# Kernel optimization log

Measured on AMD Instinct MI355X. Metric: run time of the kernel, lower is better.

Reference implementation:

```python
import jax, jax.numpy as jnp
import numpy as np

N = 8192
H = 64
ALPHA = 0.2
NEG_INF = -9e15


def gru_cell(x, h, w_ih, w_hh, b_ih, b_hh):
    # PyTorch GRUCell: gates ordered (r, z, n)
    gi = x @ w_ih.T + b_ih  # [N, 3H]
    gh = h @ w_hh.T + b_hh
    ir, iz, inn = jnp.split(gi, 3, axis=1)
    hr, hz, hn = jnp.split(gh, 3, axis=1)
    r = jax.nn.sigmoid(ir + hr)
    z = jax.nn.sigmoid(iz + hz)
    n = jnp.tanh(inn + r * hn)
    return (1.0 - z) * n + z * h


def gat(h, node_adj, edge_adj, W, a):
    hw = h @ W  # [N, H]
    h_plus = (node_adj > 0).astype(hw.dtype) @ hw
    h_minus = (node_adj < 0).astype(hw.dtype) @ hw
    # a: [2H, 1] -> per-row scalar scores
    e_plus = jax.nn.leaky_relu(jnp.concatenate([h_plus, h_minus], axis=1) @ a, ALPHA)   # [N,1]
    e_minus = jax.nn.leaky_relu(jnp.concatenate([h_minus, h_plus], axis=1) @ a, ALPHA)  # [N,1]
    # broadcast [N,1] over columns == torch .repeat(1, N)
    att = jnp.where(edge_adj > 0, e_plus, NEG_INF)
    att = jnp.where(edge_adj < 0, e_minus, att)
    att = jax.nn.softmax(att, axis=1)
    return (att * edge_adj) @ hw  # concat=False -> no elu


def setup_inputs() -> dict:
    key = jax.random.key(0)
    ks = jax.random.split(key, 12)
    f32 = jnp.float32
    inp = {
        "h": jax.random.normal(ks[0], (N, H), f32),
        "node_adj": jax.random.normal(ks[1], (N, N), f32),
        "edge_adj": jax.random.normal(ks[2], (N, N), f32),
        # GAT params
        "W_gat": jax.random.normal(ks[3], (H, H), f32) * (1.414 * np.sqrt(6.0 / (2 * H))),
        "a_gat": jax.random.normal(ks[4], (2 * H, 1), f32) * (1.414 * np.sqrt(6.0 / (2 * H + 1))),
        # edge GRU (msg_type='concat' -> input 2H)
        "w_ih_e": jax.random.normal(ks[5], (3 * H, 2 * H), f32) * 0.01,
        "w_hh_e": jax.random.normal(ks[6], (3 * H, H), f32) * 0.01,
        "b_ih_e": jnp.zeros((3 * H,), f32),
        "b_hh_e": jnp.zeros((3 * H,), f32),
        # node GRU
        "w_ih_n": jax.random.normal(ks[7], (3 * H, H), f32) * 0.01,
        "w_hh_n": jax.random.normal(ks[8], (3 * H, H), f32) * 0.01,
        "b_ih_n": jnp.zeros((3 * H,), f32),
        "b_hh_n": jnp.zeros((3 * H,), f32),
    }
    return inp


def reference(h, node_adj, edge_adj, W_gat, a_gat,
              w_ih_e, w_hh_e, b_ih_e, b_hh_e,
              w_ih_n, w_hh_n, b_ih_n, b_hh_n):
    d_node = jnp.diag(node_adj)  # diag(I_node)
    d_edge = jnp.diag(edge_adj)
    A_node = node_adj - jnp.diag(d_node)  # node_adj - I_node
    A_edge = edge_adj - jnp.diag(d_edge)
    # msg_type == 'concat'
    node_support = jnp.concatenate(
        [(A_node > 0).astype(h.dtype) @ h, (A_node < 0).astype(h.dtype) @ h], axis=1)
    edge_output = gru_cell(node_support, h, w_ih_e, w_hh_e, b_ih_e, b_hh_e)
    edge_support = gat(h, A_node, A_edge, W_gat, a_gat)
    node_output = gru_cell(edge_support, h, w_ih_n, w_hh_n, b_ih_n, b_hh_n)
    # mm with diagonal matrices == row scaling
    return d_edge[:, None] * edge_output + d_node[:, None] * node_output
```

## Files before the change

kernel.cpp:

```cpp
#include <hip/hip_runtime.h>

#define NN 8192
#define HH 64
constexpr float LALPHA = 0.2f;

typedef __attribute__((ext_vector_type(8))) short bf16x8;
typedef __attribute__((ext_vector_type(4))) float f32x4;

__device__ inline short f2bf(float f) {
  unsigned u = __builtin_bit_cast(unsigned, f);
  u += 0x7FFFu + ((u >> 16) & 1u);
  return (short)(u >> 16);
}

__global__ __launch_bounds__(256) void k_prep(const float* __restrict__ h,
                                              const float* __restrict__ na,
                                              const float* __restrict__ ea,
                                              unsigned short* __restrict__ ht,
                                              float* __restrict__ dn,
                                              float* __restrict__ de,
                                              float* __restrict__ HbP) {
  __shared__ float tile[64][65];
  const int j0 = blockIdx.x * 64;
  for (int l = threadIdx.x; l < 64 * 64; l += 256) {
    int r = l >> 6, c = l & 63;
    tile[r][c] = h[(size_t)(j0 + r) * HH + c];
  }
  __syncthreads();
  for (int l = threadIdx.x; l < 64 * 64; l += 256) {
    int c = l >> 6, r = l & 63;
    ht[(size_t)c * NN + j0 + r] = (unsigned short)f2bf(tile[r][c]);
  }
  const int t = threadIdx.x;
  if (t < 64) {
    float s = 0.f;
    for (int r = 0; r < 64; ++r) s += tile[r][t];
    HbP[blockIdx.x * 64 + t] = s;
  } else if (t < 128) {
    int i = j0 + (t - 64);
    dn[i] = na[(size_t)i * NN + i];
    de[i] = ea[(size_t)i * NN + i];
  }
}

__global__ __launch_bounds__(256) void k_wprep(
    const float* __restrict__ W, const float* __restrict__ ag,
    const float* __restrict__ wihe, const float* __restrict__ whhe,
    const float* __restrict__ wihn, const float* __restrict__ whhn,
    const float* __restrict__ HbP, float* __restrict__ Hb,
    float* __restrict__ wa0, float* __restrict__ wa1,
    float* __restrict__ wihTe, float* __restrict__ whhTe,
    float* __restrict__ WnT, float* __restrict__ whhTn) {
  const int bid = blockIdx.x, t = threadIdx.x;
  if (bid == 64) {
    __shared__ float sW[64][64];
    __shared__ float sa[128];
    for (int l = t; l < 4096; l += 256) sW[l >> 6][l & 63] = W[l];
    if (t < 128) sa[t] = ag[t];
    __syncthreads();
    if (t < 64) {
      float s0 = 0.f, s1 = 0.f;
      for (int j = 0; j < 64; ++j) {
        s0 += sW[t][j] * sa[j];
        s1 += sW[t][j] * sa[64 + j];
      }
      wa0[t] = s0;
      wa1[t] = s1;
    } else if (t < 128) {
      int c = t - 64;
      float s = 0.f;
      for (int b = 0; b < 128; ++b) s += HbP[b * 64 + c];
      Hb[c] = s;
    }
    return;
  }
  for (int x = bid * 256 + t; x < 49152; x += 64 * 256) {
    if (x < 24576) {
      int k = x / 192, g = x % 192;
      wihTe[x] = wihe[g * 128 + k];
    } else if (x < 36864) {
      int o = x - 24576, k = o / 192, g = o % 192;
      whhTe[o] = whhe[g * 64 + k];
    } else {
      int o = x - 36864, k = o / 192, g = o % 192;
      whhTn[o] = whhn[g * 64 + k];
    }
  }
  if (bid < 48) {
    const int o = bid * 256 + t;
    const int k = o / 192, g = o % 192;
    float s = 0.f;
    for (int j = 0; j < 64; ++j) s += wihn[g * 64 + j] * W[k * 64 + j];
    WnT[o] = s;
  }
}

template <int KS>
__global__ __launch_bounds__(256, 4) void k_stageA(
    const float* __restrict__ na, const float* __restrict__ ea,
    const unsigned short* __restrict__ ht,
    float* __restrict__ SpP, float* __restrict__ TfP,
    float* __restrict__ TpP, float* __restrict__ cpP) {
  const int lane  = threadIdx.x & 63;
  const int wid   = threadIdx.x >> 6;
  const int row16 = lane & 15;
  const int kgrp  = lane >> 4;
  const int i0    = blockIdx.x * 64 + wid * 16;
  const int ks    = blockIdx.y;
  const int kbeg  = ks * (NN / KS);
  constexpr int ITERS = NN / KS / 32;
  const int start = blockIdx.x & (ITERS - 1);

  f32x4 accS[4] = {}, accF[4] = {}, accP[4] = {};
  float cnt = 0.f;

  const float* naRow = na + (size_t)(i0 + row16) * NN;
  const float* eaRow = ea + (size_t)(i0 + row16) * NN;

  for (int it = 0; it < ITERS; ++it) {
    int tt = start + it;
    if (tt >= ITERS) tt -= ITERS;
    const int kk = kbeg + tt * 32 + kgrp * 8;
    const float4 a0 = *reinterpret_cast<const float4*>(naRow + kk);
    const float4 a1 = *reinterpret_cast<const float4*>(naRow + kk + 4);
    const float4 e0 = *reinterpret_cast<const float4*>(eaRow + kk);
    const float4 e1 = *reinterpret_cast<const float4*>(eaRow + kk + 4);
    const float av[8] = {a0.x, a0.y, a0.z, a0.w, a1.x, a1.y, a1.z, a1.w};
    const float ev[8] = {e0.x, e0.y, e0.z, e0.w, e1.x, e1.y, e1.z, e1.w};
    bf16x8 fS, fF, fP;
#pragma unroll
    for (int q = 0; q < 8; ++q) {
      fS[q] = (av[q] > 0.f) ? (short)0x3F80 : (short)0;
      fF[q] = f2bf(ev[q]);
      fP[q] = f2bf(fmaxf(ev[q], 0.f));
      cnt += (ev[q] > 0.f) ? 1.f : 0.f;
    }
#pragma unroll
    for (int c = 0; c < 4; ++c) {
      const bf16x8 fB = *reinterpret_cast<const bf16x8*>(
          ht + (size_t)(c * 16 + row16) * NN + kk);
      accS[c] = __builtin_amdgcn_mfma_f32_16x16x32_bf16(fS, fB, accS[c], 0, 0, 0);
      accF[c] = __builtin_amdgcn_mfma_f32_16x16x32_bf16(fF, fB, accF[c], 0, 0, 0);
      accP[c] = __builtin_amdgcn_mfma_f32_16x16x32_bf16(fP, fB, accP[c], 0, 0, 0);
    }
  }
  cnt += __shfl_xor(cnt, 16);
  cnt += __shfl_xor(cnt, 32);
  if (lane < 16) cpP[ks * NN + i0 + lane] = cnt;

  const size_t base = (size_t)ks * ((size_t)NN * HH);
#pragma unroll
  for (int c = 0; c < 4; ++c) {
#pragma unroll
    for (int r = 0; r < 4; ++r) {
      const int row = i0 + kgrp * 4 + r;
      const int col = c * 16 + row16;
      const size_t idx = base + (size_t)row * HH + col;
      SpP[idx] = accS[c][r];
      TfP[idx] = accF[c][r];
      TpP[idx] = accP[c][r];
    }
  }
}

template <int KSP>
__global__ __launch_bounds__(256) void k_epi(
    const float* __restrict__ h, const float* __restrict__ dn_g,
    const float* __restrict__ de_g, const float* __restrict__ Hb,
    const float* __restrict__ SpP, const float* __restrict__ TfP,
    const float* __restrict__ TpP, const float* __restrict__ cpP,
    const float* __restrict__ wa0, const float* __restrict__ wa1,
    const float* __restrict__ wihTe, const float* __restrict__ whhTe,
    const float* __restrict__ bihe, const float* __restrict__ bhhe,
    const float* __restrict__ WnT, const float* __restrict__ whhTn,
    const float* __restrict__ bihn, const float* __restrict__ bhhn,
    float* __restrict__ out) {
  __shared__ float xs[16][128];
  __shared__ float hs[16][64];
  __shared__ float us[16][64];
  __shared__ float eos[16][64];
  __shared__ float sHb[64], sw0[64], sw1[64];
  const int t = threadIdx.x;
  const int lane = t & 63, w = t >> 6;
  const int i0 = blockIdx.x * 16;
  const size_t SZ = (size_t)NN * HH;

  if (t < 64) {
    sHb[t] = Hb[t];
    sw0[t] = wa0[t];
    sw1[t] = wa1[t];
  }
  {
    const int row = t >> 4, c4 = (t & 15) * 4;
    *reinterpret_cast<float4*>(&hs[row][c4]) =
        *reinterpret_cast<const float4*>(&h[(size_t)(i0 + row) * 64 + c4]);
  }
  __syncthreads();

  for (int rr = 0; rr < 4; ++rr) {
    const int row = w * 4 + rr;
    const size_t idx = (size_t)(i0 + row) * 64 + lane;
    float sp = 0.f, tf = 0.f, tp = 0.f;
#pragma unroll
    for (int s = 0; s < KSP; ++s) {
      sp += SpP[s * SZ + idx];
      tf += TfP[s * SZ + idx];
      tp += TpP[s * SZ + idx];
    }
    const float hv = hs[row][lane];
    const float dni = dn_g[i0 + row], dei = de_g[i0 + row];
    sp -= (dni > 0.f) ? hv : 0.f;
    tf -= dei * hv;
    tp -= fmaxf(dei, 0.f) * hv;
    const float sm = sHb[lane] - hv - sp;
    const float tm = tf - tp;
    float cp = 0.f;
#pragma unroll
    for (int s = 0; s < KSP; ++s) cp += cpP[s * NN + i0 + row];
    cp -= (dei > 0.f) ? 1.f : 0.f;
    float ep = sp * sw0[lane] + sm * sw1[lane];
    float em = sm * sw0[lane] + sp * sw1[lane];
#pragma unroll
    for (int off = 32; off >= 1; off >>= 1) {
      ep += __shfl_xor(ep, off);
      em += __shfl_xor(em, off);
    }
    ep = ep > 0.f ? ep : LALPHA * ep;
    em = em > 0.f ? em : LALPHA * em;
    const float cm = (float)(NN - 1) - cp;
    const float NEGI = -3.0e38f;
    const float m = fmaxf(cp > 0.f ? ep : NEGI, cm > 0.f ? em : NEGI);
    const float xp = (cp > 0.f) ? expf(ep - m) : 0.f;
    const float xm = (cm > 0.f) ? expf(em - m) : 0.f;
    const float den = cp * xp + cm * xm;
    const float inv = den > 0.f ? 1.f / den : 0.f;
    xs[row][lane] = sp;
    xs[row][64 + lane] = sm;
    us[row][lane] = xp * inv * tp + xm * inv * tm;
  }
  __syncthreads();

  {
    const int c = lane;
    float gi[3][4] = {}, gh[3][4] = {};
    for (int k = 0; k < 128; ++k) {
      const float wr = wihTe[k * 192 + c], wz = wihTe[k * 192 + 64 + c],
                  wn = wihTe[k * 192 + 128 + c];
#pragma unroll
      for (int rr = 0; rr < 4; ++rr) {
        const float x = xs[w * 4 + rr][k];
        gi[0][rr] += x * wr;
        gi[1][rr] += x * wz;
        gi[2][rr] += x * wn;
      }
    }
    for (int k = 0; k < 64; ++k) {
      const float ur = whhTe[k * 192 + c], uz = whhTe[k * 192 + 64 + c],
                  un = whhTe[k * 192 + 128 + c];
#pragma unroll
      for (int rr = 0; rr < 4; ++rr) {
        const float hv = hs[w * 4 + rr][k];
        gh[0][rr] += hv * ur;
        gh[1][rr] += hv * uz;
        gh[2][rr] += hv * un;
      }
    }
    const float br = bihe[c], bz = bihe[64 + c], bn = bihe[128 + c];
    const float dr = bhhe[c], dz = bhhe[64 + c], dnb = bhhe[128 + c];
#pragma unroll
    for (int rr = 0; rr < 4; ++rr) {
      const int row = w * 4 + rr;
      const float rg = 1.f / (1.f + expf(-(gi[0][rr] + br + gh[0][rr] + dr)));
      const float zg = 1.f / (1.f + expf(-(gi[1][rr] + bz + gh[1][rr] + dz)));
      const float ng = tanhf(gi[2][rr] + bn + rg * (gh[2][rr] + dnb));
      eos[row][c] = (1.f - zg) * ng + zg * hs[row][c];
    }
  }
  __syncthreads();

  {
    const int c = lane;
    float gi[3][4] = {}, gh[3][4] = {};
    for (int k = 0; k < 64; ++k) {
      const float wr = WnT[k * 192 + c], wz = WnT[k * 192 + 64 + c],
                  wn = WnT[k * 192 + 128 + c];
      const float ur = whhTn[k * 192 + c], uz = whhTn[k * 192 + 64 + c],
                  un = whhTn[k * 192 + 128 + c];
#pragma unroll
      for (int rr = 0; rr < 4; ++rr) {
        const float x = us[w * 4 + rr][k], hv = hs[w * 4 + rr][k];
        gi[0][rr] += x * wr;
        gi[1][rr] += x * wz;
        gi[2][rr] += x * wn;
        gh[0][rr] += hv * ur;
        gh[1][rr] += hv * uz;
        gh[2][rr] += hv * un;
      }
    }
    const float br = bihn[c], bz = bihn[64 + c], bn = bihn[128 + c];
    const float dr = bhhn[c], dz = bhhn[64 + c], dnb = bhhn[128 + c];
#pragma unroll
    for (int rr = 0; rr < 4; ++rr) {
      const int row = w * 4 + rr;
      const float rg = 1.f / (1.f + expf(-(gi[0][rr] + br + gh[0][rr] + dr)));
      const float zg = 1.f / (1.f + expf(-(gi[1][rr] + bz + gh[1][rr] + dz)));
      const float ng = tanhf(gi[2][rr] + bn + rg * (gh[2][rr] + dnb));
      const float no = (1.f - zg) * ng + zg * hs[row][c];
      out[(size_t)(i0 + row) * 64 + c] =
          de_g[i0 + row] * eos[row][c] + dn_g[i0 + row] * no;
    }
  }
}

template <int KSP>
static void launch_all(const float* h, const float* na, const float* ea,
                       const float* Wg, const float* ag, const float* wihe,
                       const float* whhe, const float* bihe, const float* bhhe,
                       const float* wihn, const float* whhn, const float* bihn,
                       const float* bhhn, float* out, float* ws,
                       hipStream_t stream) {
  const size_t SZ = (size_t)NN * HH;
  float* SpP = ws;
  float* TfP = ws + (size_t)KSP * SZ;
  float* TpP = ws + (size_t)2 * KSP * SZ;
  float* cpP = ws + (size_t)3 * KSP * SZ;
  float* dn = cpP + (size_t)KSP * NN;
  float* de = dn + NN;
  float* HbP = de + NN;
  float* Hb = HbP + 8192;
  float* wa0 = Hb + 64;
  float* wa1 = wa0 + 64;
  float* wihTe = wa1 + 64;
  float* whhTe = wihTe + 24576;
  float* WnT = whhTe + 12288;
  float* whhTn = WnT + 12288;
  unsigned short* ht = (unsigned short*)(whhTn + 12288);

  k_prep<<<NN / 64, 256, 0, stream>>>(h, na, ea, ht, dn, de, HbP);
  k_wprep<<<65, 256, 0, stream>>>(Wg, ag, wihe, whhe, wihn, whhn, HbP, Hb, wa0,
                                  wa1, wihTe, whhTe, WnT, whhTn);
  k_stageA<KSP><<<dim3(NN / 64, KSP), 256, 0, stream>>>(na, ea, ht, SpP, TfP,
                                                        TpP, cpP);
  k_epi<KSP><<<NN / 16, 256, 0, stream>>>(h, dn, de, Hb, SpP, TfP, TpP, cpP,
                                          wa0, wa1, wihTe, whhTe, bihe, bhhe,
                                          WnT, whhTn, bihn, bhhn, out);
}

extern "C" void kernel_launch(void* const* d_in, const int* in_sizes, int n_in,
                              void* d_out, int out_size, void* d_ws, size_t ws_size,
                              hipStream_t stream) {
  const float* h    = (const float*)d_in[0];
  const float* na   = (const float*)d_in[1];
  const float* ea   = (const float*)d_in[2];
  const float* Wg   = (const float*)d_in[3];
  const float* ag   = (const float*)d_in[4];
  const float* wihe = (const float*)d_in[5];
  const float* whhe = (const float*)d_in[6];
  const float* bihe = (const float*)d_in[7];
  const float* bhhe = (const float*)d_in[8];
  const float* wihn = (const float*)d_in[9];
  const float* whhn = (const float*)d_in[10];
  const float* bihn = (const float*)d_in[11];
  const float* bhhn = (const float*)d_in[12];
  float* out = (float*)d_out;
  float* ws  = (float*)d_ws;

  const size_t SZ = (size_t)NN * HH;
  auto need = [&](int ks) {
    return (3 * (size_t)ks * SZ + (size_t)ks * NN + 2 * NN + 8192 + 192 +
            24576 + 3 * 12288) * 4 + (size_t)NN * HH * 2;
  };
  if (ws_size >= need(8)) {
    launch_all<8>(h, na, ea, Wg, ag, wihe, whhe, bihe, bhhe, wihn, whhn,
                  bihn, bhhn, out, ws, stream);
  } else if (ws_size >= need(4)) {
    launch_all<4>(h, na, ea, Wg, ag, wihe, whhe, bihe, bhhe, wihn, whhn,
                  bihn, bhhn, out, ws, stream);
  } else {
    launch_all<2>(h, na, ea, Wg, ag, wihe, whhe, bihe, bhhe, wihn, whhn,
                  bihn, bhhn, out, ws, stream);
  }
}
```

Measured before the change: 225.7 us.

## Precompress adjacency into bitmask and bf16 before the MFMA stage

Adds a pre-pass kernel that turns node_adj into a 1-bit sign mask and edge_adj into bf16, and counts positive edges per row with atomics. The main MFMA stage then reads the compressed operands and no longer converts fp32 per element. A fallback path keeps fp32 inputs but switches to an atomic positive-count buffer. The aim is to take conversion work out of the matmul loop, but the pre-pass adds a full extra read of both matrices plus roughly 136MB of writes and re-reads per call.

```diff
diff --git a/kernel.cpp b/kernel.cpp
--- a/kernel.cpp
+++ b/kernel.cpp
@@ -19,7 +19,8 @@
                                               unsigned short* __restrict__ ht,
                                               float* __restrict__ dn,
                                               float* __restrict__ de,
-                                              float* __restrict__ HbP) {
+                                              float* __restrict__ HbP,
+                                              int* __restrict__ cpI) {
   __shared__ float tile[64][65];
   const int j0 = blockIdx.x * 64;
   for (int l = threadIdx.x; l < 64 * 64; l += 256) {
@@ -36,10 +37,55 @@
     float s = 0.f;
     for (int r = 0; r < 64; ++r) s += tile[r][t];
     HbP[blockIdx.x * 64 + t] = s;
+    cpI[j0 + t] = 0;
   } else if (t < 128) {
     int i = j0 + (t - 64);
     dn[i] = na[(size_t)i * NN + i];
     de[i] = ea[(size_t)i * NN + i];
+    cpI[j0 + (t - 64) + 0] = 0;
+  }
+  if (t < 64) {  }
+  else if (t >= 192) { cpI[j0 + (t - 192)] = 0; }
+}
+
+__global__ __launch_bounds__(256) void k_prep2(const float* __restrict__ na,
+                                               const float* __restrict__ ea,
+                                               unsigned char* __restrict__ mask,
+                                               unsigned short* __restrict__ ebf,
+                                               int* __restrict__ cpI) {
+  const long long NG = (long long)NN * NN / 8;
+  const int half = gridDim.x >> 1;
+  const bool isNA = (int)blockIdx.x < half;
+  const long long b0 = (long long)(isNA ? blockIdx.x : blockIdx.x - half);
+  const long long stride = (long long)half * 256;
+  for (long long g = b0 * 256 + threadIdx.x; g < NG; g += stride) {
+    if (isNA) {
+      const f32x4 v0 = *reinterpret_cast<const f32x4*>(na + g * 8);
+      const f32x4 v1 = *reinterpret_cast<const f32x4*>(na + g * 8 + 4);
+      unsigned m = 0;
+#pragma unroll
+      for (int q = 0; q < 4; ++q) {
+        m |= (v0[q] > 0.f) ? (1u << q) : 0u;
+        m |= (v1[q] > 0.f) ? (1u << (q + 4)) : 0u;
+      }
+      mask[g] = (unsigned char)m;
+    } else {
+      const f32x4 v0 = *reinterpret_cast<const f32x4*>(ea + g * 8);
+      const f32x4 v1 = *reinterpret_cast<const f32x4*>(ea + g * 8 + 4);
+      bf16x8 o;
+      int tot = 0;
+#pragma unroll
+      for (int q = 0; q < 4; ++q) {
+        o[q] = f2bf(v0[q]);
+        o[q + 4] = f2bf(v1[q]);
+        tot += (v0[q] > 0.f) ? 1 : 0;
+        tot += (v1[q] > 0.f) ? 1 : 0;
+      }
+      *reinterpret_cast<bf16x8*>(ebf + g * 8) = o;
+#pragma unroll
+      for (int off = 32; off >= 1; off >>= 1) tot += __shfl_xor(tot, off);
+      if ((threadIdx.x & 63) == 0) atomicAdd(&cpI[(int)(g >> 10)], tot);
+    }
   }
 }
 
@@ -96,11 +142,10 @@
 }
 
 template <int KS>
-__global__ __launch_bounds__(256, 4) void k_stageA(
-    const float* __restrict__ na, const float* __restrict__ ea,
+__global__ __launch_bounds__(256, 4) void k_stageB(
+    const unsigned char* __restrict__ mask, const unsigned short* __restrict__ ebf,
     const unsigned short* __restrict__ ht,
-    float* __restrict__ SpP, float* __restrict__ TfP,
-    float* __restrict__ TpP, float* __restrict__ cpP) {
+    float* __restrict__ SpP, float* __restrict__ TfP, float* __restrict__ TpP) {
   const int lane  = threadIdx.x & 63;
   const int wid   = threadIdx.x >> 6;
   const int row16 = lane & 15;
@@ -112,29 +157,23 @@
   const int start = blockIdx.x & (ITERS - 1);
 
   f32x4 accS[4] = {}, accF[4] = {}, accP[4] = {};
-  float cnt = 0.f;
-
-  const float* naRow = na + (size_t)(i0 + row16) * NN;
-  const float* eaRow = ea + (size_t)(i0 + row16) * NN;
+
+  const unsigned char* mRow = mask + (size_t)(i0 + row16) * (NN / 8) + (kbeg >> 3) + kgrp;
+  const unsigned short* eRow = ebf + (size_t)(i0 + row16) * NN + kbeg + kgrp * 8;
 
   for (int it = 0; it < ITERS; ++it) {
     int tt = start + it;
     if (tt >= ITERS) tt -= ITERS;
+    const unsigned mb = mRow[tt * 4];
+    const bf16x8 fF = *reinterpret_cast<const bf16x8*>(eRow + tt * 32);
+    bf16x8 fS, fP;
+#pragma unroll
+    for (int q = 0; q < 8; ++q) {
+      fS[q] = ((mb >> q) & 1u) ? (short)0x3F80 : (short)0;
+      const short sv = fF[q];
+      fP[q] = (sv > 0) ? sv : (short)0;
+    }
     const int kk = kbeg + tt * 32 + kgrp * 8;
-    const float4 a0 = *reinterpret_cast<const float4*>(naRow + kk);
-    const float4 a1 = *reinterpret_cast<const float4*>(naRow + kk + 4);
-    const float4 e0 = *reinterpret_cast<const float4*>(eaRow + kk);
-    const float4 e1 = *reinterpret_cast<const float4*>(eaRow + kk + 4);
-    const float av[8] = {a0.x, a0.y, a0.z, a0.w, a1.x, a1.y, a1.z, a1.w};
-    const float ev[8] = {e0.x, e0.y, e0.z, e0.w, e1.x, e1.y, e1.z, e1.w};
-    bf16x8 fS, fF, fP;
-#pragma unroll
-    for (int q = 0; q < 8; ++q) {
-      fS[q] = (av[q] > 0.f) ? (short)0x3F80 : (short)0;
-      fF[q] = f2bf(ev[q]);
-      fP[q] = f2bf(fmaxf(ev[q], 0.f));
-      cnt += (ev[q] > 0.f) ? 1.f : 0.f;
-    }
 #pragma unroll
     for (int c = 0; c < 4; ++c) {
       const bf16x8 fB = *reinterpret_cast<const bf16x8*>(
@@ -144,9 +183,6 @@
       accP[c] = __builtin_amdgcn_mfma_f32_16x16x32_bf16(fP, fB, accP[c], 0, 0, 0);
     }
   }
-  cnt += __shfl_xor(cnt, 16);
-  cnt += __shfl_xor(cnt, 32);
-  if (lane < 16) cpP[ks * NN + i0 + lane] = cnt;
 
   const size_t base = (size_t)ks * ((size_t)NN * HH);
 #pragma unroll
@@ -168,7 +204,7 @@
     const float* __restrict__ h, const float* __restrict__ dn_g,
     const float* __restrict__ de_g, const float* __restrict__ Hb,
     const float* __restrict__ SpP, const float* __restrict__ TfP,
-    const float* __restrict__ TpP, const float* __restrict__ cpP,
+    const float* __restrict__ TpP, const int* __restrict__ cpI,
     const float* __restrict__ wa0, const float* __restrict__ wa1,
     const float* __restrict__ wihTe, const float* __restrict__ whhTe,
     const float* __restrict__ bihe, const float* __restrict__ bhhe,
@@ -214,9 +250,7 @@
     tp -= fmaxf(dei, 0.f) * hv;
     const float sm = sHb[lane] - hv - sp;
     const float tm = tf - tp;
-    float cp = 0.f;
-#pragma unroll
-    for (int s = 0; s < KSP; ++s) cp += cpP[s * NN + i0 + row];
+    float cp = (float)cpI[i0 + row];
     cp -= (dei > 0.f) ? 1.f : 0.f;
     float ep = sp * sw0[lane] + sm * sw1[lane];
     float em = sm * sw0[lane] + sp * sw1[lane];
@@ -312,38 +346,116 @@
   }
 }
 
-template <int KSP>
-static void launch_all(const float* h, const float* na, const float* ea,
-                       const float* Wg, const float* ag, const float* wihe,
-                       const float* whhe, const float* bihe, const float* bhhe,
-                       const float* wihn, const float* whhn, const float* bihn,
-                       const float* bhhn, float* out, float* ws,
-                       hipStream_t stream) {
+template <int KS>
+__global__ __launch_bounds__(256, 4) void k_stageAf(
+    const float* __restrict__ na, const float* __restrict__ ea,
+    const unsigned short* __restrict__ ht,
+    float* __restrict__ SpP, float* __restrict__ TfP,
+    float* __restrict__ TpP, int* __restrict__ cpI) {
+  const int lane  = threadIdx.x & 63;
+  const int wid   = threadIdx.x >> 6;
+  const int row16 = lane & 15;
+  const int kgrp  = lane >> 4;
+  const int i0    = blockIdx.x * 64 + wid * 16;
+  const int ks    = blockIdx.y;
+  const int kbeg  = ks * (NN / KS);
+  constexpr int ITERS = NN / KS / 32;
+  const int start = blockIdx.x & (ITERS - 1);
+
+  f32x4 accS[4] = {}, accF[4] = {}, accP[4] = {};
+  float cnt = 0.f;
+  const float* naRow = na + (size_t)(i0 + row16) * NN;
+  const float* eaRow = ea + (size_t)(i0 + row16) * NN;
+
+  for (int it = 0; it < ITERS; ++it) {
+    int tt = start + it;
+    if (tt >= ITERS) tt -= ITERS;
+    const int kk = kbeg + tt * 32 + kgrp * 8;
+    const float4 a0 = *reinterpret_cast<const float4*>(naRow + kk);
+    const float4 a1 = *reinterpret_cast<const float4*>(naRow + kk + 4);
+    const float4 e0 = *reinterpret_cast<const float4*>(eaRow + kk);
+    const float4 e1 = *reinterpret_cast<const float4*>(eaRow + kk + 4);
+    const float av[8] = {a0.x, a0.y, a0.z, a0.w, a1.x, a1.y, a1.z, a1.w};
+    const float ev[8] = {e0.x, e0.y, e0.z, e0.w, e1.x, e1.y, e1.z, e1.w};
+    bf16x8 fS, fF, fP;
+#pragma unroll
+    for (int q = 0; q < 8; ++q) {
+      fS[q] = (av[q] > 0.f) ? (short)0x3F80 : (short)0;
+      fF[q] = f2bf(ev[q]);
+      fP[q] = f2bf(fmaxf(ev[q], 0.f));
+      cnt += (ev[q] > 0.f) ? 1.f : 0.f;
+    }
+#pragma unroll
+    for (int c = 0; c < 4; ++c) {
+      const bf16x8 fB = *reinterpret_cast<const bf16x8*>(
+          ht + (size_t)(c * 16 + row16) * NN + kk);
+      accS[c] = __builtin_amdgcn_mfma_f32_16x16x32_bf16(fS, fB, accS[c], 0, 0, 0);
+      accF[c] = __builtin_amdgcn_mfma_f32_16x16x32_bf16(fF, fB, accF[c], 0, 0, 0);
+      accP[c] = __builtin_amdgcn_mfma_f32_16x16x32_bf16(fP, fB, accP[c], 0, 0, 0);
+    }
+  }
+  cnt += __shfl_xor(cnt, 16);
+  cnt += __shfl_xor(cnt, 32);
+  if (lane < 16) atomicAdd(&cpI[i0 + lane], (int)cnt);
+
+  const size_t base = (size_t)ks * ((size_t)NN * HH);
+#pragma unroll
+  for (int c = 0; c < 4; ++c) {
+#pragma unroll
+    for (int r = 0; r < 4; ++r) {
+      const int row = i0 + kgrp * 4 + r;
+      const int col = c * 16 + row16;
+      const size_t idx = base + (size_t)row * HH + col;
+      SpP[idx] = accS[c][r];
+      TfP[idx] = accF[c][r];
+      TpP[idx] = accP[c][r];
+    }
+  }
+}
+
+struct WsLayout {
+  float *SpP, *TfP, *TpP, *dn, *de, *HbP, *Hb, *wa0, *wa1, *wihTe, *whhTe, *WnT, *whhTn;
+  int* cpI;
+  unsigned short* ht;
+  unsigned char* mask;
+  unsigned short* ebf;
+};
+
+static WsLayout carve(void* ws, int KS) {
   const size_t SZ = (size_t)NN * HH;
-  float* SpP = ws;
-  float* TfP = ws + (size_t)KSP * SZ;
-  float* TpP = ws + (size_t)2 * KSP * SZ;
-  float* cpP = ws + (size_t)3 * KSP * SZ;
-  float* dn = cpP + (size_t)KSP * NN;
-  float* de = dn + NN;
-  float* HbP = de + NN;
-  float* Hb = HbP + 8192;
-  float* wa0 = Hb + 64;
-  float* wa1 = wa0 + 64;
-  float* wihTe = wa1 + 64;
-  float* whhTe = wihTe + 24576;
-  float* WnT = whhTe + 12288;
-  float* whhTn = WnT + 12288;
-  unsigned short* ht = (unsigned short*)(whhTn + 12288);
-
-  k_prep<<<NN / 64, 256, 0, stream>>>(h, na, ea, ht, dn, de, HbP);
-  k_wprep<<<65, 256, 0, stream>>>(Wg, ag, wihe, whhe, wihn, whhn, HbP, Hb, wa0,
-                                  wa1, wihTe, whhTe, WnT, whhTn);
-  k_stageA<KSP><<<dim3(NN / 64, KSP), 256, 0, stream>>>(na, ea, ht, SpP, TfP,
-                                                        TpP, cpP);
-  k_epi<KSP><<<NN / 16, 256, 0, stream>>>(h, dn, de, Hb, SpP, TfP, TpP, cpP,
-                                          wa0, wa1, wihTe, whhTe, bihe, bhhe,
-                                          WnT, whhTn, bihn, bhhn, out);
+  uintptr_t p = (uintptr_t)ws;
+  auto take = [&](size_t bytes) {
+    uintptr_t r = (p + 255) & ~(uintptr_t)255;
+    p = r + bytes;
+    return r;
+  };
+  WsLayout L;
+  L.SpP = (float*)take(KS * SZ * 4);
+  L.TfP = (float*)take(KS * SZ * 4);
+  L.TpP = (float*)take(KS * SZ * 4);
+  L.dn = (float*)take(NN * 4);
+  L.de = (float*)take(NN * 4);
+  L.HbP = (float*)take(8192 * 4);
+  L.Hb = (float*)take(64 * 4);
+  L.wa0 = (float*)take(64 * 4);
+  L.wa1 = (float*)take(64 * 4);
+  L.wihTe = (float*)take(24576 * 4);
+  L.whhTe = (float*)take(12288 * 4);
+  L.WnT = (float*)take(12288 * 4);
+  L.whhTn = (float*)take(12288 * 4);
+  L.cpI = (int*)take(NN * 4);
+  L.ht = (unsigned short*)take((size_t)NN * 64 * 2);
+  L.mask = (unsigned char*)take((size_t)NN * NN / 8);
+  L.ebf = (unsigned short*)take((size_t)NN * NN * 2);
+  return L;
+}
+
+static size_t needBytes(int KS, bool compressed) {
+  const size_t SZ = (size_t)NN * HH;
+  size_t s = 3 * KS * SZ * 4 + NN * 8 + 8192 * 4 + 64 * 12 + 61440 * 4 + NN * 4 +
+             (size_t)NN * 64 * 2 + 17 * 256;
+  if (compressed) s += (size_t)NN * NN / 8 + (size_t)NN * NN * 2;
+  return s;
 }
 
 extern "C" void kernel_launch(void* const* d_in, const int* in_sizes, int n_in,
@@ -363,21 +475,35 @@
   const float* bihn = (const float*)d_in[11];
   const float* bhhn = (const float*)d_in[12];
   float* out = (float*)d_out;
-  float* ws  = (float*)d_ws;
-
-  const size_t SZ = (size_t)NN * HH;
-  auto need = [&](int ks) {
-    return (3 * (size_t)ks * SZ + (size_t)ks * NN + 2 * NN + 8192 + 192 +
-            24576 + 3 * 12288) * 4 + (size_t)NN * HH * 2;
-  };
-  if (ws_size >= need(8)) {
-    launch_all<8>(h, na, ea, Wg, ag, wihe, whhe, bihe, bhhe, wihn, whhn,
-                  bihn, bhhn, out, ws, stream);
-  } else if (ws_size >= need(4)) {
-    launch_all<4>(h, na, ea, Wg, ag, wihe, whhe, bihe, bhhe, wihn, whhn,
-                  bihn, bhhn, out, ws, stream);
+
+  const bool c8 = ws_size >= needBytes(8, true);
+  const bool c4 = !c8 && ws_size >= needBytes(4, true);
+  const int KS = (c8 || !c4) ? 8 : 4;
+  WsLayout L = carve(d_ws, KS);
+
+  k_prep<<<NN / 64, 256, 0, stream>>>(h, na, ea, L.ht, L.dn, L.de, L.HbP, L.cpI);
+  k_wprep<<<65, 256, 0, stream>>>(Wg, ag, wihe, whhe, wihn, whhn, L.HbP, L.Hb,
+                                  L.wa0, L.wa1, L.wihTe, L.whhTe, L.WnT, L.whhTn);
+  if (c8 || c4) {
+    k_prep2<<<2048, 256, 0, stream>>>(na, ea, L.mask, L.ebf, L.cpI);
+    if (c8)
+      k_stageB<8><<<dim3(NN / 64, 8), 256, 0, stream>>>(L.mask, L.ebf, L.ht,
+                                                        L.SpP, L.TfP, L.TpP);
+    else
+      k_stageB<4><<<dim3(NN / 64, 4), 256, 0, stream>>>(L.mask, L.ebf, L.ht,
+                                                        L.SpP, L.TfP, L.TpP);
   } else {
-    launch_all<2>(h, na, ea, Wg, ag, wihe, whhe, bihe, bhhe, wihn, whhn,
-                  bihn, bhhn, out, ws, stream);
-  }
-}
+    k_stageAf<8><<<dim3(NN / 64, 8), 256, 0, stream>>>(na, ea, L.ht, L.SpP,
+                                                       L.TfP, L.TpP, L.cpI);
+  }
+  if (c4)
+    k_epi<4><<<NN / 16, 256, 0, stream>>>(h, L.dn, L.de, L.Hb, L.SpP, L.TfP,
+                                          L.TpP, L.cpI, L.wa0, L.wa1, L.wihTe,
+                                          L.whhTe, bihe, bhhe, L.WnT, L.whhTn,
+                                          bihn, bhhn, out);
+  else
+    k_epi<8><<<NN / 16, 256, 0, stream>>>(h, L.dn, L.de, L.Hb, L.SpP, L.TfP,
+                                          L.TpP, L.cpI, L.wa0, L.wa1, L.wihTe,
+                                          L.whhTe, bihe, bhhe, L.WnT, L.whhTn,
+                                          bihn, bhhn, out);
+}
```

Measured after the change: 313.5 us. 38.9% more time.
